# Kernel optimization log

Measured on AMD Instinct MI355X. Metric: run time of the kernel, lower is better.

## Reference

```python
import jax, jax.numpy as jnp
import numpy as np

N_NODES = 40000
N_EDGES = 150000
H, D = 4, 128  # heads, per-head dim (h_feats=512)


def _edge_softmax(e, dst, n):
    # e: [E, H] attention logits; softmax over edges sharing a dst node
    m = jax.ops.segment_max(e, dst, num_segments=n)
    w = jnp.exp(e - m[dst])
    s = jax.ops.segment_sum(w, dst, num_segments=n)
    return w / s[dst]


def _gat_conv(x, src, dst, W, al, ar, b, activate):
    # DGL GATConv: feat = x @ W -> [N, H, D]
    n = x.shape[0]
    feat = (x @ W).reshape(n, H, D)
    el = jnp.einsum('nhd,hd->nh', feat, al)  # [N, H]
    er = jnp.einsum('nhd,hd->nh', feat, ar)
    e = jax.nn.leaky_relu(el[src] + er[dst], negative_slope=0.2)  # [E, H]
    a = _edge_softmax(e, dst, n)
    msg = feat[src] * a[:, :, None]  # [E, H, D]
    out = jax.ops.segment_sum(msg, dst, num_segments=n)  # [N, H, D]
    out = out + b.reshape(1, H, D)
    if activate:
        out = jax.nn.leaky_relu(out, negative_slope=0.01)  # F.leaky_relu default
    return out


def _hetero_layer(h, edges, W, al, ar, b, activate):
    # HeteroGraphConv with aggregate='sum' over edge types, then flatten heads
    n = h.shape[0]
    out = jnp.zeros((n, H, D), h.dtype)
    for t, (src, dst) in enumerate(edges):
        out = out + _gat_conv(h, src, dst, W[t], al[t], ar[t], b[t], activate)
    return out.reshape(n, H * D)


def setup_inputs() -> dict:
    key = jax.random.key(0)
    ks = jax.random.split(key, 20)
    inp = {}
    inp['x'] = jax.random.normal(ks[0], (N_NODES, 1024), jnp.float32)
    for i, nm in enumerate(['src0', 'dst0', 'src1', 'dst1']):
        inp[nm] = jax.random.randint(ks[1 + i], (N_EDGES,), 0, N_NODES, jnp.int32)
    def wscale(k, shape, fan_in):
        return jax.random.normal(k, shape, jnp.float32) * (1.0 / np.sqrt(fan_in))
    inp['W0'] = wscale(ks[5], (2, 1024, 512), 1024)
    inp['al0'] = wscale(ks[6], (2, H, D), D)
    inp['ar0'] = wscale(ks[7], (2, H, D), D)
    inp['b0'] = jnp.zeros((2, 512), jnp.float32)
    inp['W1'] = wscale(ks[8], (2, 512, 512), 512)
    inp['al1'] = wscale(ks[9], (2, H, D), D)
    inp['ar1'] = wscale(ks[10], (2, H, D), D)
    inp['b1'] = jnp.zeros((2, 512), jnp.float32)
    inp['W2'] = wscale(ks[11], (2, 512, 512), 512)
    inp['al2'] = wscale(ks[12], (2, H, D), D)
    inp['ar2'] = wscale(ks[13], (2, H, D), D)
    inp['b2'] = jnp.zeros((2, 512), jnp.float32)
    inp['Wout'] = wscale(ks[14], (512, 2983), 512)
    inp['bout'] = jnp.zeros((2983,), jnp.float32)
    return inp


def reference(x, src0, dst0, src1, dst1,
              W0, al0, ar0, b0, W1, al1, ar1, b1, W2, al2, ar2, b2,
              Wout, bout):
    edges = [(src0, dst0), (src1, dst1)]
    h = _hetero_layer(x, edges, W0, al0, ar0, b0, activate=True)
    h = _hetero_layer(h, edges, W1, al1, ar1, b1, activate=True)
    h = _hetero_layer(h, edges, W2, al2, ar2, b2, activate=False)
    return h @ Wout + bout
```

## Files before the change

### kernel.cpp

```cpp
#include <hip/hip_runtime.h>
#include <hip/hip_bf16.h>

#define NN 40000
#define NE 150000
#define HF 512
#define NHEAD 4

typedef __bf16 bf16x8 __attribute__((ext_vector_type(8)));
typedef float floatx4 __attribute__((ext_vector_type(4)));
typedef __hip_bfloat16 bf16;
typedef unsigned short u16;

__device__ __forceinline__ float bf2f(bf16 v) { return __bfloat162float(v); }

__device__ __forceinline__ void gload16(const void* g, void* l) {
    __builtin_amdgcn_global_load_lds(
        (const __attribute__((address_space(1))) void*)g,
        (__attribute__((address_space(3))) void*)l, 16, 0, 0);
}

__global__ void cast_k(const float* __restrict__ in, bf16* __restrict__ out, int n) {
    int i = (blockIdx.x * blockDim.x + threadIdx.x) * 8;
    if (i + 7 < n) {
        float4 v0 = *(const float4*)(in + i);
        float4 v1 = *(const float4*)(in + i + 4);
        union { uint4 u; u16 s[8]; } w;
        float fv[8] = {v0.x, v0.y, v0.z, v0.w, v1.x, v1.y, v1.z, v1.w};
#pragma unroll
        for (int j = 0; j < 8; j++) {
            bf16 b = __float2bfloat16(fv[j]);
            w.s[j] = *(const u16*)&b;
        }
        *(uint4*)(out + i) = w.u;
    } else {
        for (int j = i; j < n; j++) out[j] = __float2bfloat16(in[j]);
    }
}

__global__ void transpose_k(const float* __restrict__ W, bf16* __restrict__ WT,
                            int K, int Nn) {
    __shared__ float tile[32][33];
    int n0 = blockIdx.x * 32, k0 = blockIdx.y * 32;
    int tx = threadIdx.x, ty = threadIdx.y;
    int n = n0 + tx, k = k0 + ty;
    if (n < Nn && k < K) tile[ty][tx] = W[(size_t)k * Nn + n];
    __syncthreads();
    int nn = n0 + ty, kk = k0 + tx;
    if (nn < Nn && kk < K) WT[(size_t)nn * K + kk] = __float2bfloat16(tile[tx][ty]);
}

template <bool HAS_BIAS>
__global__ __launch_bounds__(256) void gemm_k(const bf16* __restrict__ A,
                                              const bf16* __restrict__ BT,
                                              float* __restrict__ C,
                                              const float* __restrict__ bias,
                                              int M, int Nn, int K) {
    __shared__ __align__(16) unsigned short As[128][32];
    __shared__ __align__(16) unsigned short Bs[128][32];

    const int nwg = gridDim.x * gridDim.y;
    const int orig = blockIdx.y * gridDim.x + blockIdx.x;
    const int qq = nwg >> 3, r8 = nwg & 7;
    const int xcd = orig & 7, loc = orig >> 3;
    const int swz = (xcd < r8 ? xcd * (qq + 1) : r8 * (qq + 1) + (xcd - r8) * qq) + loc;
    const int ntile = swz % gridDim.x;
    const int mtile = swz / gridDim.x;
    const int m0 = mtile * 128;
    const int n0 = ntile * 128;

    const int t = threadIdx.x;
    const int lane = t & 63;
    const int wave = t >> 6;
    const int wm = wave >> 1, wn = wave & 1;
    const int q = lane >> 4, r = lane & 15;

    const int srow = wave * 32 + (lane >> 2);
    const int scol = (lane & 3) * 8;
    int ar0 = m0 + srow;        if (ar0 >= M)  ar0 = M - 1;
    int ar1 = m0 + srow + 16;   if (ar1 >= M)  ar1 = M - 1;
    int br0 = n0 + srow;        if (br0 >= Nn) br0 = Nn - 1;
    int br1 = n0 + srow + 16;   if (br1 >= Nn) br1 = Nn - 1;
    const unsigned short* Ag0 = (const unsigned short*)A + (size_t)ar0 * K + scol;
    const unsigned short* Ag1 = (const unsigned short*)A + (size_t)ar1 * K + scol;
    const unsigned short* Bg0 = (const unsigned short*)BT + (size_t)br0 * K + scol;
    const unsigned short* Bg1 = (const unsigned short*)BT + (size_t)br1 * K + scol;
    unsigned short* Al0 = &As[0][0] + wave * 1024;
    unsigned short* Al1 = Al0 + 512;
    unsigned short* Bl0 = &Bs[0][0] + wave * 1024;
    unsigned short* Bl1 = Bl0 + 512;

    floatx4 acc[4][4] = {};
    for (int k0 = 0; k0 < K; k0 += 32) {
        gload16(Ag0 + k0, Al0);
        gload16(Ag1 + k0, Al1);
        gload16(Bg0 + k0, Bl0);
        gload16(Bg1 + k0, Bl1);
        __syncthreads();
        bf16x8 a[4], b[4];
#pragma unroll
        for (int i = 0; i < 4; i++) a[i] = *(const bf16x8*)&As[wm * 64 + i * 16 + r][q * 8];
#pragma unroll
        for (int j = 0; j < 4; j++) b[j] = *(const bf16x8*)&Bs[wn * 64 + j * 16 + r][q * 8];
#pragma unroll
        for (int i = 0; i < 4; i++)
#pragma unroll
            for (int j = 0; j < 4; j++)
                acc[i][j] = __builtin_amdgcn_mfma_f32_16x16x32_bf16(a[i], b[j], acc[i][j], 0, 0, 0);
        __syncthreads();
    }
#pragma unroll
    for (int i = 0; i < 4; i++)
#pragma unroll
        for (int j = 0; j < 4; j++)
#pragma unroll
            for (int rr = 0; rr < 4; rr++) {
                int row = m0 + wm * 64 + i * 16 + q * 4 + rr;
                int col = n0 + wn * 64 + j * 16 + r;
                if (row < M && col < Nn) {
                    float v = acc[i][j][rr];
                    if (HAS_BIAS) v += bias[col];
                    C[(size_t)row * Nn + col] = v;
                }
            }
}

__global__ void attn_k(const float* __restrict__ feat, const float* __restrict__ al,
                       const float* __restrict__ ar, float* __restrict__ el,
                       float* __restrict__ er) {
    int lane = threadIdx.x & 63;
    int wave = threadIdx.x >> 6;
    int node = blockIdx.x * 4 + wave;
    if (node >= NN) return;
    int h = lane >> 4;
    const float* fp = feat + (size_t)node * HF + lane * 8;
    float4 f0 = *(const float4*)fp;
    float4 f1 = *(const float4*)(fp + 4);
    const float* alp = al + h * 128 + (lane & 15) * 8;
    const float* arp = ar + h * 128 + (lane & 15) * 8;
    float fv[8] = {f0.x, f0.y, f0.z, f0.w, f1.x, f1.y, f1.z, f1.w};
    float sl = 0.f, sr = 0.f;
#pragma unroll
    for (int j = 0; j < 8; j++) {
        sl += fv[j] * alp[j];
        sr += fv[j] * arp[j];
    }
#pragma unroll
    for (int off = 8; off >= 1; off >>= 1) {
        sl += __shfl_down(sl, off, 16);
        sr += __shfl_down(sr, off, 16);
    }
    if ((lane & 15) == 0) {
        el[node * NHEAD + h] = sl;
        er[node * NHEAD + h] = sr;
    }
}

__global__ void deg_count_k(const int* __restrict__ dst, int* __restrict__ deg) {
    int e = blockIdx.x * blockDim.x + threadIdx.x;
    if (e < NE) atomicAdd(&deg[dst[e]], 1);
}

__global__ void scan_k(const int* __restrict__ deg, int* __restrict__ off) {
    __shared__ int part[1024];
    const int CH = (NN + 1023) >> 10;
    int t = threadIdx.x;
    int base = t * CH;
    int s = 0;
    for (int i = 0; i < CH; i++) {
        int idx = base + i;
        if (idx < NN) s += deg[idx];
    }
    part[t] = s;
    __syncthreads();
    for (int d = 1; d < 1024; d <<= 1) {
        int v = (t >= d) ? part[t - d] : 0;
        __syncthreads();
        part[t] += v;
        __syncthreads();
    }
    int run = (t == 0) ? 0 : part[t - 1];
    for (int i = 0; i < CH; i++) {
        int idx = base + i;
        if (idx < NN) {
            off[idx] = run;
            run += deg[idx];
        } else if (idx == NN) {
            off[NN] = run;
        }
    }
}

__global__ void fill_k(const int* __restrict__ src, const int* __restrict__ dst,
                       const int* __restrict__ off, int* __restrict__ cur,
                       int* __restrict__ csrc) {
    int e = blockIdx.x * blockDim.x + threadIdx.x;
    if (e >= NE) return;
    int d = dst[e];
    int p = atomicAdd(&cur[d], 1);
    csrc[off[d] + p] = src[e];
}

__global__ __launch_bounds__(256) void gather_k(
    const int* __restrict__ off, const int* __restrict__ csrc,
    const float* __restrict__ el, const float* __restrict__ er,
    const float* __restrict__ feat, const float* __restrict__ bt,
    bf16* __restrict__ hout, int first, int act) {
    int lane = threadIdx.x & 63;
    int wave = threadIdx.x >> 6;
    int d = blockIdx.x * 4 + wave;
    if (d >= NN) return;
    int h = lane >> 4;
    int o0 = off[d], o1 = off[d + 1];
    float erd = er[d * NHEAD + h];

    float m = -3.0e38f, sum = 0.f;
    for (int i = o0; i < o1; i++) {
        int s = csrc[i];
        float lg = el[s * NHEAD + h] + erd;
        lg = lg > 0.f ? lg : 0.2f * lg;
        float mn = fmaxf(m, lg);
        sum = sum * __expf(m - mn) + __expf(lg - mn);
        m = mn;
    }
    float inv = sum > 0.f ? 1.f / sum : 0.f;
    float acc[8] = {};
    for (int i = o0; i < o1; i++) {
        int s = csrc[i];
        float lg = el[s * NHEAD + h] + erd;
        lg = lg > 0.f ? lg : 0.2f * lg;
        float a = __expf(lg - m) * inv;
        const float* fp = feat + (size_t)s * HF + lane * 8;
        float4 f0 = *(const float4*)fp;
        float4 f1 = *(const float4*)(fp + 4);
        acc[0] += f0.x * a;
        acc[1] += f0.y * a;
        acc[2] += f0.z * a;
        acc[3] += f0.w * a;
        acc[4] += f1.x * a;
        acc[5] += f1.y * a;
        acc[6] += f1.z * a;
        acc[7] += f1.w * a;
    }
    const float* bp = bt + lane * 8;
    float4 b0 = *(const float4*)bp;
    float4 b1 = *(const float4*)(bp + 4);
    float bv[8] = {b0.x, b0.y, b0.z, b0.w, b1.x, b1.y, b1.z, b1.w};
    u16* hp = (u16*)(hout + (size_t)d * HF + lane * 8);
    union U8 { uint4 v; u16 s[8]; };
    U8 prev;
    if (!first) prev.v = *(const uint4*)hp;
    U8 outw;
#pragma unroll
    for (int j = 0; j < 8; j++) {
        float v = acc[j] + bv[j];
        if (act) v = v > 0.f ? v : 0.01f * v;
        if (!first) {
            bf16 pb = *(const bf16*)&prev.s[j];
            v += bf2f(pb);
        }
        bf16 ob = __float2bfloat16(v);
        outw.s[j] = *(const u16*)&ob;
    }
    *(uint4*)hp = outw.v;
}

extern "C" void kernel_launch(void* const* d_in, const int* in_sizes, int n_in,
                              void* d_out, int out_size, void* d_ws, size_t ws_size,
                              hipStream_t stream) {
    const float* x = (const float*)d_in[0];
    const int* srcs[2] = {(const int*)d_in[1], (const int*)d_in[3]};
    const int* dsts[2] = {(const int*)d_in[2], (const int*)d_in[4]};
    const float* W[3] = {(const float*)d_in[5], (const float*)d_in[9], (const float*)d_in[13]};
    const float* al[3] = {(const float*)d_in[6], (const float*)d_in[10], (const float*)d_in[14]};
    const float* ar[3] = {(const float*)d_in[7], (const float*)d_in[11], (const float*)d_in[15]};
    const float* bb[3] = {(const float*)d_in[8], (const float*)d_in[12], (const float*)d_in[16]};
    const float* Wout = (const float*)d_in[17];
    const float* bout = (const float*)d_in[18];

    char* ws = (char*)d_ws;
    size_t off = 0;
    auto walloc = [&](size_t bytes) {
        void* p = ws + off;
        off = (off + bytes + 255) & ~(size_t)255;
        return p;
    };
    bf16* h0 = (bf16*)walloc((size_t)NN * HF * 2);
    bf16* h1 = (bf16*)walloc((size_t)NN * HF * 2);
    float* feat = (float*)walloc((size_t)NN * HF * 4);
    float* el = (float*)walloc((size_t)NN * NHEAD * 4);
    float* er = (float*)walloc((size_t)NN * NHEAD * 4);
    bf16* WT = (bf16*)walloc((size_t)2983 * 512 * 2);
    int* deg = (int*)walloc((size_t)NN * 4);
    int* cur = (int*)walloc((size_t)NN * 4);
    int* offs[2];
    int* csrc[2];
    for (int t = 0; t < 2; t++) {
        offs[t] = (int*)walloc((size_t)(NN + 1) * 4);
        csrc[t] = (int*)walloc((size_t)NE * 4);
    }

    bf16* xb = (bf16*)((char*)d_out + (size_t)NN * HF * 4);

    cast_k<<<(NN * 1024 / 8 + 255) / 256, 256, 0, stream>>>(x, xb, NN * 1024);

    const int EB = (NE + 255) / 256;
    for (int t = 0; t < 2; t++) {
        hipMemsetAsync(deg, 0, (size_t)NN * 4, stream);
        hipMemsetAsync(cur, 0, (size_t)NN * 4, stream);
        deg_count_k<<<EB, 256, 0, stream>>>(dsts[t], deg);
        scan_k<<<1, 1024, 0, stream>>>(deg, offs[t]);
        fill_k<<<EB, 256, 0, stream>>>(srcs[t], dsts[t], offs[t], cur, csrc[t]);
    }

    const int MT = (NN + 127) / 128;

    for (int l = 0; l < 3; l++) {
        const int K = (l == 0) ? 1024 : 512;
        const bf16* hin = (l == 0) ? xb : ((l == 1) ? h0 : h1);
        bf16* hout = (l == 0) ? h0 : ((l == 1) ? h1 : h0);
        const int act = (l < 2) ? 1 : 0;
        for (int t = 0; t < 2; t++) {
            transpose_k<<<dim3(512 / 32, K / 32), dim3(32, 32), 0, stream>>>(
                W[l] + (size_t)t * K * 512, WT, K, 512);
            gemm_k<false><<<dim3(512 / 128, MT), 256, 0, stream>>>(
                hin, WT, feat, nullptr, NN, 512, K);
            attn_k<<<NN / 4, 256, 0, stream>>>(feat, al[l] + t * HF, ar[l] + t * HF, el, er);
            gather_k<<<NN / 4, 256, 0, stream>>>(offs[t], csrc[t], el, er, feat,
                                                 bb[l] + t * HF, hout, t == 0 ? 1 : 0, act);
        }
    }

    transpose_k<<<dim3((2983 + 31) / 32, 512 / 32), dim3(32, 32), 0, stream>>>(
        Wout, WT, 512, 2983);
    gemm_k<true><<<dim3((2983 + 127) / 128, MT), 256, 0, stream>>>(
        h0, WT, (float*)d_out, bout, NN, 2983, 512);
}
```

Baseline: 1.764 ms.

## Double-buffer GEMM LDS tiles with async prefetch and XOR-swizzled layout

```diff
diff --git a/kernel.cpp b/kernel.cpp
--- a/kernel.cpp
+++ b/kernel.cpp
@@ -17,6 +17,10 @@
     __builtin_amdgcn_global_load_lds(
         (const __attribute__((address_space(1))) void*)g,
         (__attribute__((address_space(3))) void*)l, 16, 0, 0);
+}
+
+__device__ __forceinline__ void wait_vm0() {
+    asm volatile("s_waitcnt vmcnt(0)" ::: "memory");
 }
 
 __global__ void cast_k(const float* __restrict__ in, bf16* __restrict__ out, int n) {
@@ -55,8 +59,8 @@
                                               float* __restrict__ C,
                                               const float* __restrict__ bias,
                                               int M, int Nn, int K) {
-    __shared__ __align__(16) unsigned short As[128][32];
-    __shared__ __align__(16) unsigned short Bs[128][32];
+    __shared__ __align__(16) unsigned short As[2][128][32];
+    __shared__ __align__(16) unsigned short Bs[2][128][32];
 
     const int nwg = gridDim.x * gridDim.y;
     const int orig = blockIdx.y * gridDim.x + blockIdx.x;
@@ -75,7 +79,7 @@
     const int q = lane >> 4, r = lane & 15;
 
     const int srow = wave * 32 + (lane >> 2);
-    const int scol = (lane & 3) * 8;
+    const int scol = ((lane & 3) ^ ((srow >> 1) & 3)) * 8;
     int ar0 = m0 + srow;        if (ar0 >= M)  ar0 = M - 1;
     int ar1 = m0 + srow + 16;   if (ar1 >= M)  ar1 = M - 1;
     int br0 = n0 + srow;        if (br0 >= Nn) br0 = Nn - 1;
@@ -84,29 +88,52 @@
     const unsigned short* Ag1 = (const unsigned short*)A + (size_t)ar1 * K + scol;
     const unsigned short* Bg0 = (const unsigned short*)BT + (size_t)br0 * K + scol;
     const unsigned short* Bg1 = (const unsigned short*)BT + (size_t)br1 * K + scol;
-    unsigned short* Al0 = &As[0][0] + wave * 1024;
-    unsigned short* Al1 = Al0 + 512;
-    unsigned short* Bl0 = &Bs[0][0] + wave * 1024;
-    unsigned short* Bl1 = Bl0 + 512;
+    unsigned short* Alb[2] = {&As[0][0][0] + wave * 1024, &As[1][0][0] + wave * 1024};
+    unsigned short* Blb[2] = {&Bs[0][0][0] + wave * 1024, &Bs[1][0][0] + wave * 1024};
+
+    const int rchunk = (q ^ ((r >> 1) & 3)) * 8;
 
     floatx4 acc[4][4] = {};
-    for (int k0 = 0; k0 < K; k0 += 32) {
-        gload16(Ag0 + k0, Al0);
-        gload16(Ag1 + k0, Al1);
-        gload16(Bg0 + k0, Bl0);
-        gload16(Bg1 + k0, Bl1);
-        __syncthreads();
+    const int nt = K >> 5;
+    int cur = 0;
+    gload16(Ag0, Alb[0]);
+    gload16(Ag1, Alb[0] + 512);
+    gload16(Bg0, Blb[0]);
+    gload16(Bg1, Blb[0] + 512);
+    wait_vm0();
+    __syncthreads();
+    for (int tt = 0; tt < nt; tt++) {
+        if (tt + 1 < nt) {
+            const int k1 = (tt + 1) << 5;
+            gload16(Ag0 + k1, Alb[cur ^ 1]);
+            gload16(Ag1 + k1, Alb[cur ^ 1] + 512);
+            gload16(Bg0 + k1, Blb[cur ^ 1]);
+            gload16(Bg1 + k1, Blb[cur ^ 1] + 512);
+        }
         bf16x8 a[4], b[4];
 #pragma unroll
-        for (int i = 0; i < 4; i++) a[i] = *(const bf16x8*)&As[wm * 64 + i * 16 + r][q * 8];
-#pragma unroll
-        for (int j = 0; j < 4; j++) b[j] = *(const bf16x8*)&Bs[wn * 64 + j * 16 + r][q * 8];
+        for (int i = 0; i < 4; i++)
+            a[i] = *(const bf16x8*)&As[cur][wm * 64 + i * 16 + r][rchunk];
+#pragma unroll
+        for (int j = 0; j < 4; j++)
+            b[j] = *(const bf16x8*)&Bs[cur][wn * 64 + j * 16 + r][rchunk];
 #pragma unroll
         for (int i = 0; i < 4; i++)
 #pragma unroll
             for (int j = 0; j < 4; j++)
                 acc[i][j] = __builtin_amdgcn_mfma_f32_16x16x32_bf16(a[i], b[j], acc[i][j], 0, 0, 0);
+        wait_vm0();
         __syncthreads();
+        cur ^= 1;
+    }
+
+    float bv4[4] = {0.f, 0.f, 0.f, 0.f};
+    if (HAS_BIAS) {
+#pragma unroll
+        for (int j = 0; j < 4; j++) {
+            int col = n0 + wn * 64 + j * 16 + r;
+            if (col < Nn) bv4[j] = bias[col];
+        }
     }
 #pragma unroll
     for (int i = 0; i < 4; i++)
@@ -118,7 +145,7 @@
                 int col = n0 + wn * 64 + j * 16 + r;
                 if (row < M && col < Nn) {
                     float v = acc[i][j][rr];
-                    if (HAS_BIAS) v += bias[col];
+                    if (HAS_BIAS) v += bv4[j];
                     C[(size_t)row * Nn + col] = v;
                 }
             }
```

After: 1.700 ms. 1.04x faster.
